# Kernel tuning notes

Hardware: AMD Instinct MI355X
Metric: run time of the kernel (lower is better)

Reference implementation:

```python
import math
import jax, jax.numpy as jnp
import numpy as np

P = 0.5        # dropout probability
Q = 1.0        # internal exponent = q/2 with q=2.0


def setup_inputs() -> dict:
    key = jax.random.key(0)
    k1, k2, k3 = jax.random.split(key, 3)
    bS, inF, outF = 256, 1024, 1024
    stdv = 1.0 / math.sqrt(inF)
    x = jax.random.normal(k1, (bS, inF), dtype=jnp.float32)
    weight = jax.random.uniform(k2, (inF, outF), dtype=jnp.float32, minval=-stdv, maxval=stdv)
    bias = jax.random.uniform(k3, (outF,), dtype=jnp.float32, minval=-stdv, maxval=stdv)
    return {"x": x, "weight": weight, "bias": bias}


def reference(x, weight, bias):
    # Training path of BridgeoutFcLayer (batch_mask=False): per-sample noise.
    bS = x.shape[0]
    # noise = bernoulli(1-p)/(1-p) - 1  -> values {p/(1-p), -1}; detached constant.
    keep = jax.random.bernoulli(jax.random.key(42), 1.0 - P, (bS,) + weight.shape)
    noise = keep.astype(weight.dtype) / (1.0 - P) - 1.0  # (bS, in, out)
    # perturbed per-sample weight: w + |w|^(q/2) * noise
    w = weight + jnp.abs(weight) ** Q * noise  # (bS, in, out)
    out = jnp.einsum('bi,bio->bo', x, w) + bias  # (bS, out)
    return out
```

## Files before the change

kernel.cpp:

```cpp
#include <hip/hip_runtime.h>
#include <stdint.h>


#define TFR2(sh) \
  "v_add_u32 %[a0], %[a0], %[a1]\n\t" \
  "v_add_u32 %[b0], %[b0], %[b1]\n\t" \
  "v_alignbit_b32 %[a1], %[a1], %[a1], " #sh "\n\t" \
  "v_alignbit_b32 %[b1], %[b1], %[b1], " #sh "\n\t" \
  "v_xor_b32 %[a1], %[a1], %[a0]\n\t" \
  "v_xor_b32 %[b1], %[b1], %[b0]\n\t"

__device__ __forceinline__ void tf_dual(uint32_t& a0, uint32_t& b0) {
  uint32_t a1, b1;
  asm(
      "v_alignbit_b32 %[a1], %[a0], %[a0], 19\n\t"
      "v_alignbit_b32 %[b1], %[b0], %[b0], 19\n\t"
      "v_xor_b32 %[a1], %[a1], %[a0]\n\t"
      "v_xor_b32 %[b1], %[b1], %[b0]\n\t"
      TFR2(17) TFR2(6) TFR2(26)
      "v_add_u32 %[a0], 42, %[a0]\n\t"
      "v_add_u32 %[b0], 42, %[b0]\n\t"
      "v_add_u32 %[a1], 0x1bd11bf1, %[a1]\n\t"
      "v_add_u32 %[b1], 0x1bd11bf1, %[b1]\n\t"
      TFR2(15) TFR2(3) TFR2(16) TFR2(8)
      "v_add_u32 %[a0], 0x1bd11bf0, %[a0]\n\t"
      "v_add_u32 %[b0], 0x1bd11bf0, %[b0]\n\t"
      "v_add_u32 %[a1], 2, %[a1]\n\t"
      "v_add_u32 %[b1], 2, %[b1]\n\t"
      TFR2(19) TFR2(17) TFR2(6) TFR2(26)
      "v_add_u32 %[a1], 45, %[a1]\n\t"
      "v_add_u32 %[b1], 45, %[b1]\n\t"
      TFR2(15) TFR2(3) TFR2(16) TFR2(8)
      "v_add_u32 %[a0], 42, %[a0]\n\t"
      "v_add_u32 %[b0], 42, %[b0]\n\t"
      "v_add_u32 %[a1], 0x1bd11bf4, %[a1]\n\t"
      "v_add_u32 %[b1], 0x1bd11bf4, %[b1]\n\t"
      TFR2(19) TFR2(17) TFR2(6) TFR2(26)
      "v_add_u32 %[a0], 0x1bd11bf0, %[a0]\n\t"
      "v_add_u32 %[b0], 0x1bd11bf0, %[b0]\n\t"
      "v_add_u32 %[a1], 5, %[a1]\n\t"
      "v_add_u32 %[b1], 5, %[b1]\n\t"
      "v_xor_b32 %[a0], %[a0], %[a1]\n\t"
      "v_xor_b32 %[b0], %[b0], %[b1]"
      : [a0] "+v"(a0), [b0] "+v"(b0), [a1] "=&v"(a1), [b1] "=&v"(b1));
}

__device__ __forceinline__ float sign_inject(uint32_t bits, float w) {
  uint32_t r = (bits & 0x80000000u) | (__float_as_uint(w) & 0x7FFFFFFFu);
  return __uint_as_float(r);
}

__global__ __launch_bounds__(256) void BridgeoutFcLayer_60413009985793_kernel(
    const float* __restrict__ x, const float* __restrict__ weight,
    const float* __restrict__ bias, float* __restrict__ out) {
  const int oc = blockIdx.x & 3;
  const int b  = blockIdx.x >> 2;
  const int o  = (oc << 8) + threadIdx.x;

  __shared__ float xs0[1024];
  __shared__ float xs1[1024];
  for (int t = threadIdx.x; t < 1024; t += 256) {
    xs0[t] = x[t + (b << 10)];
    xs1[t] = x[t + ((b + 128) << 10)];
  }
  __syncthreads();

  float acc0 = 0.0f, acc1 = 0.0f;
  const uint32_t cbase0 = ((uint32_t)b << 20) + (uint32_t)o;
  uint32_t cbase = cbase0;
  const float* wp = weight + o;

#pragma unroll 2
  for (int i = 0; i < 1024; i += 4) {
#pragma unroll 4
    for (int u = 0; u < 4; ++u) {
      float w = wp[u << 10];
      uint32_t hA = cbase + (uint32_t)((u << 10) + 42);
      uint32_t hB = cbase + (uint32_t)((u << 10) + 42) + 0x08000000u;
      tf_dual(hA, hB);
      acc0 = fmaf(xs0[i + u], w + sign_inject(hA, w), acc0);
      acc1 = fmaf(xs1[i + u], w + sign_inject(hB, w), acc1);
    }
    cbase += 4096u;
    wp += 4096;
  }

  float bo = bias[o];
  out[(b << 10) + o]         = acc0 + bo;
  out[((b + 128) << 10) + o] = acc1 + bo;
}

extern "C" void kernel_launch(void* const* d_in, const int* in_sizes, int n_in,
                              void* d_out, int out_size, void* d_ws, size_t ws_size,
                              hipStream_t stream) {
  const float* x      = (const float*)d_in[0];
  const float* weight = (const float*)d_in[1];
  const float* bias   = (const float*)d_in[2];
  float* out          = (float*)d_out;

  BridgeoutFcLayer_60413009985793_kernel<<<512, 256, 0, stream>>>(x, weight, bias, out);
}
```

Measured before the change: 536.6 us.

## Assign one batch row per thread and double the grid size

```diff
diff --git a/kernel.cpp b/kernel.cpp
--- a/kernel.cpp
+++ b/kernel.cpp
@@ -57,37 +57,38 @@
   const int b  = blockIdx.x >> 2;
   const int o  = (oc << 8) + threadIdx.x;
 
-  __shared__ float xs0[1024];
-  __shared__ float xs1[1024];
-  for (int t = threadIdx.x; t < 1024; t += 256) {
-    xs0[t] = x[t + (b << 10)];
-    xs1[t] = x[t + ((b + 128) << 10)];
-  }
+  __shared__ float xs[1024];
+  for (int t = threadIdx.x; t < 1024; t += 256) xs[t] = x[t + (b << 10)];
   __syncthreads();
 
-  float acc0 = 0.0f, acc1 = 0.0f;
-  const uint32_t cbase0 = ((uint32_t)b << 20) + (uint32_t)o;
-  uint32_t cbase = cbase0;
+  float acc = 0.0f;
+  uint32_t cbase = ((uint32_t)b << 20) + (uint32_t)o;
   const float* wp = weight + o;
 
-#pragma unroll 2
   for (int i = 0; i < 1024; i += 4) {
-#pragma unroll 4
-    for (int u = 0; u < 4; ++u) {
-      float w = wp[u << 10];
-      uint32_t hA = cbase + (uint32_t)((u << 10) + 42);
-      uint32_t hB = cbase + (uint32_t)((u << 10) + 42) + 0x08000000u;
-      tf_dual(hA, hB);
-      acc0 = fmaf(xs0[i + u], w + sign_inject(hA, w), acc0);
-      acc1 = fmaf(xs1[i + u], w + sign_inject(hB, w), acc1);
-    }
+    float4 x4 = *reinterpret_cast<const float4*>(&xs[i]);
+    float w0 = wp[0];
+    float w1 = wp[1 << 10];
+    float w2 = wp[2 << 10];
+    float w3 = wp[3 << 10];
+
+    uint32_t h0 = cbase + 42u;
+    uint32_t h1 = cbase + (1024u + 42u);
+    uint32_t h2 = cbase + (2048u + 42u);
+    uint32_t h3 = cbase + (3072u + 42u);
+    tf_dual(h0, h1);
+    tf_dual(h2, h3);
+
+    acc = fmaf(x4.x, w0 + sign_inject(h0, w0), acc);
+    acc = fmaf(x4.y, w1 + sign_inject(h1, w1), acc);
+    acc = fmaf(x4.z, w2 + sign_inject(h2, w2), acc);
+    acc = fmaf(x4.w, w3 + sign_inject(h3, w3), acc);
+
     cbase += 4096u;
     wp += 4096;
   }
 
-  float bo = bias[o];
-  out[(b << 10) + o]         = acc0 + bo;
-  out[((b + 128) << 10) + o] = acc1 + bo;
+  out[(b << 10) + o] = acc + bias[o];
 }
 
 extern "C" void kernel_launch(void* const* d_in, const int* in_sizes, int n_in,
@@ -98,5 +99,5 @@
   const float* bias   = (const float*)d_in[2];
   float* out          = (float*)d_out;
 
-  BridgeoutFcLayer_60413009985793_kernel<<<512, 256, 0, stream>>>(x, weight, bias, out);
+  BridgeoutFcLayer_60413009985793_kernel<<<1024, 256, 0, stream>>>(x, weight, bias, out);
 }
```

Result: faster. 518.1 us (-3.4%).
